# Kernel tuning notes

Hardware: AMD Instinct MI355X
Metric: run time of the kernel (lower is better)

Reference implementation:

```python
import jax, jax.numpy as jnp
import numpy as np

N = 131072          # batch of (action, condition) pairs
ACT_D = 12          # action_dim
COND_D = 256        # condition_dim
K = 256             # num_embeddings (codebook size)
E = 16              # embedding_dim
H1, H2 = 512, 256   # encoder_hidden_dims
COMMIT = 0.25       # commitment_cost
EPS_NORM = 1e-12    # F.normalize eps


def _normalize(x):
    n = jnp.linalg.norm(x, axis=-1, keepdims=True)
    return x / jnp.maximum(n, EPS_NORM)


def setup_inputs() -> dict:
    key = jax.random.key(0)
    ks = jax.random.split(key, 16)
    s = 0.02
    return {
        "actions": jax.random.normal(ks[0], (N, ACT_D), jnp.float32),
        "conditions": jax.random.normal(ks[1], (N, COND_D), jnp.float32),
        # encoder: (COND_D+ACT_D) -> H1 -> H2 -> E  (weights stored [in, out])
        "enc_w1": jax.random.normal(ks[2], (COND_D + ACT_D, H1), jnp.float32) * s,
        "enc_b1": jnp.zeros((H1,), jnp.float32),
        "enc_w2": jax.random.normal(ks[3], (H1, H2), jnp.float32) * s,
        "enc_b2": jnp.zeros((H2,), jnp.float32),
        "enc_w3": jax.random.normal(ks[4], (H2, E), jnp.float32) * s,
        "enc_b3": jnp.zeros((E,), jnp.float32),
        # decoder: (COND_D+E) -> H2 -> H1 -> ACT_D
        "dec_w1": jax.random.normal(ks[5], (COND_D + E, H2), jnp.float32) * s,
        "dec_b1": jnp.zeros((H2,), jnp.float32),
        "dec_w2": jax.random.normal(ks[6], (H2, H1), jnp.float32) * s,
        "dec_b2": jnp.zeros((H1,), jnp.float32),
        "dec_w3": jax.random.normal(ks[7], (H1, ACT_D), jnp.float32) * s,
        "dec_b3": jnp.zeros((ACT_D,), jnp.float32),
        # codebook, init U(-1/K, 1/K) like nn.Embedding in the module
        "embedding": jax.random.uniform(ks[8], (K, E), jnp.float32, -1.0 / K, 1.0 / K),
    }


def reference(actions, conditions, enc_w1, enc_b1, enc_w2, enc_b2, enc_w3, enc_b3,
              dec_w1, dec_b1, dec_w2, dec_b2, dec_w3, dec_b3, embedding):
    sg = jax.lax.stop_gradient
    elu = jax.nn.elu

    # ---- encoder ----
    x = jnp.concatenate([actions, conditions], axis=-1)          # [N, ACT_D+COND_D]
    h = elu(x @ enc_w1 + enc_b1)
    h = elu(h @ enc_w2 + enc_b2)
    z = h @ enc_w3 + enc_b3                                      # [N, E]

    # ---- vector quantizer (distance='cos') ----
    normed_in = sg(_normalize(z))                                # inputs.detach()
    normed_w = _normalize(embedding)
    distances = normed_in @ normed_w.T                           # [N, K] cosine sims

    idx = jnp.argmax(distances, axis=-1)                         # [N]
    quantized = embedding[idx]                                   # one-hot @ codebook == gather

    e_latent_loss = COMMIT * jnp.mean((sg(quantized) - z) ** 2)
    q_latent_loss = jnp.mean((quantized - sg(z)) ** 2)
    quantized_st = z + sg(quantized - z)                         # straight-through

    counts = jnp.zeros((K,), distances.dtype).at[idx].add(1.0)
    avg_probs = counts / N                                       # mean of one-hot encodings
    perplexity = jnp.exp(-jnp.sum(avg_probs * jnp.log(avg_probs + 1e-10)))

    # ---- contrastive loss (training branch, deterministic part) ----
    sortd = jnp.sort(distances, axis=0)                          # ascending per codeword
    n_pos = max(1, N // K)
    dis_pos = jnp.mean(sortd[-n_pos:, :], axis=0, keepdims=True) # [1, K] hardest positives
    dis_neg = sortd[: N // 2, :]                                 # [N//2, K]
    dis = jnp.concatenate([dis_pos, dis_neg], axis=0).T / 0.07   # [K, 1+N//2]
    # cross-entropy with target class 0
    contra_loss = jnp.mean(jax.nn.logsumexp(dis, axis=1) - dis[:, 0])

    # ---- decoder ----
    d = jnp.concatenate([quantized_st, conditions], axis=-1)     # [N, E+COND_D]
    d = elu(d @ dec_w1 + dec_b1)
    d = elu(d @ dec_w2 + dec_b2)
    reconstructed = d @ dec_w3 + dec_b3                          # [N, ACT_D]

    reconstruction_loss = jnp.mean((reconstructed - actions) ** 2)

    return (reconstructed, quantized_st, idx.astype(jnp.int32), q_latent_loss,
            e_latent_loss, contra_loss, perplexity, reconstruction_loss)
```

## Files before the change

kernel.cpp:

```cpp
#include <hip/hip_runtime.h>
#include <hip/hip_bf16.h>
#include <math.h>

#define NROWS 131072
#define ACT_D 12
#define COND_D 256
#define KEMB 256
#define EDIM 16
#define H1D 512
#define H2D 256
#define NB 16384

typedef __attribute__((ext_vector_type(8))) _Float16 half8;
typedef __attribute__((ext_vector_type(4))) float floatx4;
typedef unsigned short ushort_t;

#define LO_SCALE 4096.0f
#define INV_LO_SCALE 2.44140625e-4f


__global__ void init_kernel(int* counts, float* outScal) {
    int t = threadIdx.x;
    counts[t] = 0;
    if (t < 5) outScal[t] = 0.0f;
}

__device__ inline ushort_t f16bits(_Float16 h) { return __builtin_bit_cast(ushort_t, h); }
__device__ inline float f16pair(ushort_t a, ushort_t b) {
    return (float)__builtin_bit_cast(_Float16, a)
         + (float)__builtin_bit_cast(_Float16, b) * INV_LO_SCALE;
}
__device__ inline void splitf(float v, ushort_t& hi, ushort_t& lo) {
    _Float16 h = (_Float16)v;
    _Float16 l = (_Float16)((v - (float)h) * LO_SCALE);
    hi = f16bits(h); lo = f16bits(l);
}

__device__ inline void gload_lds16(const void* g, void* lds) {
    __builtin_amdgcn_global_load_lds((const __attribute__((address_space(1))) void*)g,
                                     (__attribute__((address_space(3))) void*)lds, 16, 0, 0);
}

__global__ __launch_bounds__(256)
void convw_kernel(const float* __restrict__ W, ushort_t* __restrict__ Whi,
                  ushort_t* __restrict__ Wlo, int K, int N, int Kp)
{
    int n = blockIdx.x;
    int k = blockIdx.y * 256 + threadIdx.x;
    if (k >= Kp) return;
    float v = (k < K) ? W[(long)k * N + n] : 0.0f;
    ushort_t h, l; splitf(v, h, l);
    Whi[(long)n * Kp + k] = h;
    Wlo[(long)n * Kp + k] = l;
}

template<int CONCAT>
__global__ __launch_bounds__(256)
void gemm_f16x3_kernel(const void* A0v, const void* A1v,
                       const ushort_t* __restrict__ Bhi, const ushort_t* __restrict__ Blo,
                       const float* __restrict__ bias,
                       ushort_t* __restrict__ Chi, ushort_t* __restrict__ Clo,
                       int Nw, int Kp, int Kvalid)
{
    __shared__ uint lds[8192];
    const int tid = threadIdx.x;
    const int w = tid >> 6, l = tid & 63;
    const int quad = l >> 4, lr = l & 15;
    const long rowBase = (long)blockIdx.x * 128;
    const int colBase = blockIdx.y * 128;
    const int mQ = (w & 1) * 64, nQ = (w >> 1) * 64;

    floatx4 accH[4][4], accX[4][4];
#pragma unroll
    for (int i = 0; i < 4; ++i)
#pragma unroll
        for (int j = 0; j < 4; ++j) { accH[i][j] = (floatx4)(0.0f); accX[i][j] = (floatx4)(0.0f); }

    const int kTiles = Kp / 32;
    for (int t = 0; t < kTiles; ++t) {
        const int k0 = t * 32;
        {
            const ushort_t* src = (w < 2) ? Bhi : Blo;
            uint* dstBase = &lds[(w < 2) ? 4096 : 6144];
            const int j0 = (w & 1) * 4;
#pragma unroll
            for (int j = 0; j < 4; ++j) {
                int jj = j0 + j;
                const ushort_t* g = src + (long)(colBase + jj * 16 + (l >> 2)) * Kp
                                        + k0 + (l & 3) * 8;
                gload_lds16(g, &dstBase[jj * 256]);
            }
        }
        if (CONCAT == 0) {
            const ushort_t* src = (w < 2) ? (const ushort_t*)A0v : (const ushort_t*)A1v;
            uint* dstBase = &lds[(w < 2) ? 0 : 2048];
            const int j0 = (w & 1) * 4;
#pragma unroll
            for (int j = 0; j < 4; ++j) {
                int jj = j0 + j;
                const ushort_t* g = src + (rowBase + jj * 16 + (l >> 2)) * Kp
                                        + k0 + (l & 3) * 8;
                gload_lds16(g, &dstBase[jj * 256]);
            }
        } else {
            const float* A1 = (const float*)A0v;
            const float* A2 = (const float*)A1v;
            const int r = tid >> 1;
            const long grow = rowBase + r;
            const int segBase = (tid & 1) * 2;
#pragma unroll
            for (int s = 0; s < 2; ++s) {
                int seg = segBase + s;
                int kk = k0 + seg * 8;
                float v[8];
                if (kk >= CONCAT && kk + 8 <= Kvalid) {
                    const float* p = A2 + grow * COND_D + (kk - CONCAT);
                    *(float4*)&v[0] = *(const float4*)p;
                    *(float4*)&v[4] = *(const float4*)(p + 4);
                } else if (kk + 8 <= CONCAT) {
                    const float* p = A1 + grow * CONCAT + kk;
                    *(float4*)&v[0] = *(const float4*)p;
                    *(float4*)&v[4] = *(const float4*)(p + 4);
                } else {
#pragma unroll
                    for (int i = 0; i < 8; ++i) {
                        int k = kk + i;
                        v[i] = (k < CONCAT) ? A1[grow * CONCAT + k]
                             : (k < Kvalid) ? A2[grow * COND_D + (k - CONCAT)] : 0.0f;
                    }
                }
                uint hh[4], ll[4];
#pragma unroll
                for (int i = 0; i < 4; ++i) {
                    ushort_t h0, l0, h1, l1;
                    splitf(v[2 * i], h0, l0);
                    splitf(v[2 * i + 1], h1, l1);
                    hh[i] = (uint)h0 | ((uint)h1 << 16);
                    ll[i] = (uint)l0 | ((uint)l1 << 16);
                }
                int dst = r * 16 + seg * 4;
                *(uint4*)&lds[dst]        = *(uint4*)hh;
                *(uint4*)&lds[2048 + dst] = *(uint4*)ll;
            }
        }
        __syncthreads();

#pragma unroll
        for (int jn = 0; jn < 4; ++jn) {
            int boff = (nQ + jn * 16 + lr) * 16 + quad * 4;
            half8 bh = __builtin_bit_cast(half8, *(uint4*)&lds[4096 + boff]);
            half8 bl = __builtin_bit_cast(half8, *(uint4*)&lds[6144 + boff]);
#pragma unroll
            for (int im = 0; im < 4; ++im) {
                int aoff = (mQ + im * 16 + lr) * 16 + quad * 4;
                half8 ah = __builtin_bit_cast(half8, *(uint4*)&lds[aoff]);
                half8 al = __builtin_bit_cast(half8, *(uint4*)&lds[2048 + aoff]);
                accH[im][jn] = __builtin_amdgcn_mfma_f32_16x16x32_f16(ah, bh, accH[im][jn], 0, 0, 0);
                accX[im][jn] = __builtin_amdgcn_mfma_f32_16x16x32_f16(ah, bl, accX[im][jn], 0, 0, 0);
                accX[im][jn] = __builtin_amdgcn_mfma_f32_16x16x32_f16(al, bh, accX[im][jn], 0, 0, 0);
            }
        }
        __syncthreads();
    }

    float bv[4];
#pragma unroll
    for (int jn = 0; jn < 4; ++jn) bv[jn] = bias[colBase + nQ + jn * 16 + lr];
#pragma unroll
    for (int im = 0; im < 4; ++im) {
#pragma unroll
        for (int jn = 0; jn < 4; ++jn) {
            int n = colBase + nQ + jn * 16 + lr;
#pragma unroll
            for (int rr = 0; rr < 4; ++rr) {
                long m = rowBase + mQ + im * 16 + quad * 4 + rr;
                float x = accH[im][jn][rr] + accX[im][jn][rr] * INV_LO_SCALE + bv[jn];
                x = x > 0.0f ? x : (expf(x) - 1.0f);
                ushort_t h, lo; splitf(x, h, lo);
                long idx = m * Nw + n;
                Chi[idx] = h;
                Clo[idx] = lo;
            }
        }
    }
}

__global__ __launch_bounds__(256)
void quantize_kernel(const ushort_t* __restrict__ h2hi, const ushort_t* __restrict__ h2lo,
                     const float* __restrict__ W3,
                     const float* __restrict__ b3, const float* __restrict__ emb,
                     float* __restrict__ distT, float* __restrict__ outQ,
                     float* __restrict__ outIdx, int* __restrict__ counts,
                     float* __restrict__ qsum)
{
    __shared__ float h2t[16 * 260];
    __shared__ float w3t[16 * 260];
    __shared__ float nwt[256 * 20];
    __shared__ float zt[16 * 17];
    __shared__ float dt[16 * 257];
    __shared__ int   lcnt[256];
    __shared__ float swred[4];

    int t = threadIdx.x;
    long rowBase = (long)blockIdx.x * 16;

    for (int it = 0; it < 16; ++it) {
        long idx = (rowBase + it) * 256 + t;
        h2t[it * 260 + t] = f16pair(h2hi[idx], h2lo[idx]);
    }
    for (int it = 0; it < 16; ++it) {
        int flat = it * 256 + t;
        int j = flat >> 4, c = flat & 15;
        w3t[c * 260 + j] = W3[flat];
    }
    {
        float e0[16]; float ss = 0.f;
#pragma unroll
        for (int i = 0; i < 16; ++i) { e0[i] = emb[t * 16 + i]; ss += e0[i] * e0[i]; }
        float inv = 1.0f / fmaxf(sqrtf(ss), 1e-12f);
#pragma unroll
        for (int i = 0; i < 16; ++i) nwt[t * 20 + i] = e0[i] * inv;
    }
    lcnt[t] = 0;
    __syncthreads();

    int r = t >> 4, c = t & 15;
    float zacc = b3[c];
    for (int j4 = 0; j4 < 64; ++j4) {
        float4 h = *(const float4*)&h2t[r * 260 + j4 * 4];
        float4 w = *(const float4*)&w3t[c * 260 + j4 * 4];
        zacc += h.x * w.x + h.y * w.y + h.z * w.z + h.w * w.w;
    }
    float ss = zacc * zacc;
#pragma unroll
    for (int m = 1; m < 16; m <<= 1) ss += __shfl_xor(ss, m, 64);
    zt[r * 17 + c] = zacc / fmaxf(sqrtf(ss), 1e-12f);
    __syncthreads();

    float zr[16];
#pragma unroll
    for (int e = 0; e < 16; ++e) zr[e] = zt[r * 17 + e];
    float best = -1e30f; int bidx = 0;
    for (int cc = 0; cc < 16; ++cc) {
        int col = cc * 16 + c;
        float d = 0.f;
#pragma unroll
        for (int e4 = 0; e4 < 4; ++e4) {
            float4 wv = *(const float4*)&nwt[col * 20 + e4 * 4];
            d += zr[e4 * 4 + 0] * wv.x + zr[e4 * 4 + 1] * wv.y
               + zr[e4 * 4 + 2] * wv.z + zr[e4 * 4 + 3] * wv.w;
        }
        dt[r * 257 + col] = d;
        if (d > best || (d == best && col < bidx)) { best = d; bidx = col; }
    }
#pragma unroll
    for (int m = 1; m < 16; m <<= 1) {
        float ov = __shfl_xor(best, m, 64);
        int   oi = __shfl_xor(bidx, m, 64);
        if (ov > best || (ov == best && oi < bidx)) { best = ov; bidx = oi; }
    }

    float q = emb[bidx * 16 + c];
    outQ[(rowBase + r) * 16 + c] = q;
    float df = q - zacc;
    float part = df * df;
#pragma unroll
    for (int m = 1; m < 64; m <<= 1) part += __shfl_xor(part, m, 64);
    if ((t & 63) == 0) swred[t >> 6] = part;
    if (c == 0) {
        outIdx[rowBase + r] = (float)bidx;
        atomicAdd(&lcnt[bidx], 1);
    }
    __syncthreads();
    if (t == 0) atomicAdd(qsum, swred[0] + swred[1] + swred[2] + swred[3]);
    if (lcnt[t] > 0) atomicAdd(&counts[t], lcnt[t]);

    int rr = t & 15, cg = t >> 4;
    for (int i = 0; i < 16; ++i) {
        int col = i * 16 + cg;
        distT[(long)col * NROWS + rowBase + rr] = dt[rr * 257 + col];
    }
}

__global__ __launch_bounds__(1024)
void selA_kernel(const float* __restrict__ distT, int* __restrict__ stats)
{
    __shared__ int hist[NB];
    __shared__ int part[1024];
    int t = threadIdx.x, c = blockIdx.x;
    for (int i = t; i < NB; i += 1024) hist[i] = 0;
    __syncthreads();
    const float* col = distT + (long)c * NROWS;
    for (int i = t; i < NROWS; i += 1024) {
        float v = col[i];
        int b = (int)((v + 1.0f) * (NB * 0.5f));
        b = min(max(b, 0), NB - 1);
        atomicAdd(&hist[b], 1);
    }
    __syncthreads();
    const int CH = NB / 1024;
    int s = 0;
    for (int i = 0; i < CH; ++i) s += hist[t * CH + i];
    part[t] = s;
    __syncthreads();
    if (t == 0) {
        int target = NROWS / 2;
        int cum = 0; int chunk = 0;
        while (cum + part[chunk] < target) { cum += part[chunk]; ++chunk; }
        int b = chunk * CH;
        while (cum + hist[b] < target) { cum += hist[b]; ++b; }
        int medBin = b, needLow = target - cum, cntMed = hist[b];
        int cumA = 0; chunk = 1023;
        while (cumA + part[chunk] < 512) { cumA += part[chunk]; --chunk; }
        b = chunk * CH + CH - 1;
        while (cumA + hist[b] < 512) { cumA += hist[b]; --b; }
        int topBin = b, needTop = 512 - cumA, cntTop = hist[b];
        int* st = stats + c * 6;
        st[0] = medBin; st[1] = needLow; st[2] = cntMed;
        st[3] = topBin; st[4] = needTop; st[5] = cntTop;
    }
}

__global__ __launch_bounds__(1024)
void selB_kernel(const float* __restrict__ distT, const int* __restrict__ stats,
                 float* __restrict__ contra_sum)
{
    __shared__ float red[64];
    int t = threadIdx.x, c = blockIdx.x;
    const int* st = stats + c * 6;
    int medBin = st[0], needLow = st[1], cntMed = st[2];
    int topBin = st[3], needTop = st[4], cntTop = st[5];
    const float binw = 2.0f / NB;
    float mUp = -1.0f + (medBin + 1) * binw;
    const float INVT = 1.0f / 0.07f;
    const float* col = distT + (long)c * NROWS;
    float topS = 0.f, tbS = 0.f, lowS = 0.f, mbS = 0.f;
    for (int i = t; i < NROWS; i += 1024) {
        float v = col[i];
        int b = (int)((v + 1.0f) * (NB * 0.5f));
        b = min(max(b, 0), NB - 1);
        if (b > topBin)       topS += v;
        else if (b == topBin) tbS += v;
        if (b < medBin)       lowS += expf((v - mUp) * INVT);
        else if (b == medBin) mbS  += expf((v - mUp) * INVT);
    }
#pragma unroll
    for (int m = 1; m < 64; m <<= 1) {
        topS += __shfl_xor(topS, m, 64);
        tbS  += __shfl_xor(tbS, m, 64);
        lowS += __shfl_xor(lowS, m, 64);
        mbS  += __shfl_xor(mbS, m, 64);
    }
    if ((t & 63) == 0) {
        int wv = t >> 6;
        red[wv * 4 + 0] = topS; red[wv * 4 + 1] = tbS;
        red[wv * 4 + 2] = lowS; red[wv * 4 + 3] = mbS;
    }
    __syncthreads();
    if (t == 0) {
        float T0 = 0, T1 = 0, T2 = 0, T3 = 0;
        for (int wv = 0; wv < 16; ++wv) {
            T0 += red[wv * 4 + 0]; T1 += red[wv * 4 + 1];
            T2 += red[wv * 4 + 2]; T3 += red[wv * 4 + 3];
        }
        float dis_pos = (T0 + needTop * (T1 / cntTop)) * (1.0f / 512.0f);
        float S = T2 + needLow * (T3 / cntMed);
        float colContra = log1pf(S * expf((mUp - dis_pos) * INVT));
        atomicAdd(contra_sum, colContra);
    }
}

__global__ __launch_bounds__(256)
void dec3_kernel(const ushort_t* __restrict__ d2hi, const ushort_t* __restrict__ d2lo,
                 const float* __restrict__ W,
                 const float* __restrict__ bias, const float* __restrict__ actions,
                 float* __restrict__ rec, float* __restrict__ recon_sum)
{
    __shared__ float dtile[16 * 516];
    __shared__ float wt[512 * 12];
    __shared__ float red2[4];
    int t = threadIdx.x;
    long rowBase = (long)blockIdx.x * 16;
    for (int it = 0; it < 24; ++it) wt[it * 256 + t] = W[it * 256 + t];
    for (int it = 0; it < 32; ++it) {
        int flat = it * 256 + t;
        int r = flat >> 9, k = flat & 511;
        long idx = (rowBase + r) * 512 + k;
        dtile[r * 516 + k] = f16pair(d2hi[idx], d2lo[idx]);
    }
    __syncthreads();
    float part = 0.f;
    if (t < 192) {
        int r = t / 12, cc = t % 12;
        float acc = bias[cc];
        for (int k4 = 0; k4 < 128; ++k4) {
            float4 h = *(const float4*)&dtile[r * 516 + k4 * 4];
            acc += h.x * wt[(k4 * 4 + 0) * 12 + cc] + h.y * wt[(k4 * 4 + 1) * 12 + cc]
                 + h.z * wt[(k4 * 4 + 2) * 12 + cc] + h.w * wt[(k4 * 4 + 3) * 12 + cc];
        }
        rec[(rowBase + r) * 12 + cc] = acc;
        float df = acc - actions[(rowBase + r) * 12 + cc];
        part = df * df;
    }
#pragma unroll
    for (int m = 1; m < 64; m <<= 1) part += __shfl_xor(part, m, 64);
    if ((t & 63) == 0) red2[t >> 6] = part;
    __syncthreads();
    if (t == 0) atomicAdd(recon_sum, red2[0] + red2[1] + red2[2] + red2[3]);
}

__global__ void finalize_kernel(const int* __restrict__ counts, float* __restrict__ outScal)
{
    __shared__ float red[4];
    int t = threadIdx.x;
    float p = counts[t] * (1.0f / NROWS);
    float term = p * logf(p + 1e-10f);
#pragma unroll
    for (int m = 1; m < 64; m <<= 1) term += __shfl_xor(term, m, 64);
    if ((t & 63) == 0) red[t >> 6] = term;
    __syncthreads();
    if (t == 0) {
        float hsum = red[0] + red[1] + red[2] + red[3];
        float qsum = outScal[0], contra = outScal[2], recon = outScal[4];
        float ql = qsum * (1.0f / (NROWS * 16.0f));
        outScal[0] = ql;
        outScal[1] = 0.25f * ql;
        outScal[2] = contra * (1.0f / 256.0f);
        outScal[3] = expf(-hsum);
        outScal[4] = recon * (1.0f / (NROWS * 12.0f));
    }
}

extern "C" void kernel_launch(void* const* d_in, const int* in_sizes, int n_in,
                              void* d_out, int out_size, void* d_ws, size_t ws_size,
                              hipStream_t stream)
{
    const float* actions    = (const float*)d_in[0];
    const float* conditions = (const float*)d_in[1];
    const float* enc_w1 = (const float*)d_in[2];
    const float* enc_b1 = (const float*)d_in[3];
    const float* enc_w2 = (const float*)d_in[4];
    const float* enc_b2 = (const float*)d_in[5];
    const float* enc_w3 = (const float*)d_in[6];
    const float* enc_b3 = (const float*)d_in[7];
    const float* dec_w1 = (const float*)d_in[8];
    const float* dec_b1 = (const float*)d_in[9];
    const float* dec_w2 = (const float*)d_in[10];
    const float* dec_b2 = (const float*)d_in[11];
    const float* dec_w3 = (const float*)d_in[12];
    const float* dec_b3 = (const float*)d_in[13];
    const float* emb    = (const float*)d_in[14];

    float* out     = (float*)d_out;
    float* outRec  = out;
    float* outQ    = out + (long)NROWS * 12;
    float* outIdx  = out + (long)NROWS * 28;
    float* outScal = out + (long)NROWS * 29;

    ushort_t* wb    = (ushort_t*)d_out;
    ushort_t* w1hi  = wb;            ushort_t* w1lo  = wb + 147456;
    ushort_t* w2hi  = wb + 294912;   ushort_t* w2lo  = wb + 425984;
    ushort_t* wd1hi = wb + 557056;   ushort_t* wd1lo = wb + 630784;
    ushort_t* wd2hi = wb + 704512;   ushort_t* wd2lo = wb + 835584;

    float* ws = (float*)d_ws;
    int* counts = (int*)ws;
    int* stats  = (int*)(ws + 256);
    ushort_t* h2hi = (ushort_t*)(ws + 1792);
    ushort_t* h2lo = (ushort_t*)(ws + 16779008);
    ushort_t* d1hi = h2hi;
    ushort_t* d1lo = h2lo;
    float*    P1   = ws + 33556224;
    ushort_t* h1hi = (ushort_t*)P1;
    ushort_t* h1lo = (ushort_t*)(ws + 67110656);
    float*    distT = P1;
    ushort_t* d2hi = h1hi;
    ushort_t* d2lo = h1lo;

    hipLaunchKernelGGL(init_kernel, dim3(1), dim3(256), 0, stream, counts, outScal);
    hipLaunchKernelGGL(convw_kernel, dim3(512, 2), dim3(256), 0, stream, enc_w1, w1hi, w1lo, 268, 512, 288);
    hipLaunchKernelGGL(convw_kernel, dim3(256, 2), dim3(256), 0, stream, enc_w2, w2hi, w2lo, 512, 256, 512);
    hipLaunchKernelGGL(convw_kernel, dim3(256, 2), dim3(256), 0, stream, dec_w1, wd1hi, wd1lo, 272, 256, 288);
    hipLaunchKernelGGL(convw_kernel, dim3(512, 1), dim3(256), 0, stream, dec_w2, wd2hi, wd2lo, 256, 512, 256);
    hipLaunchKernelGGL((gemm_f16x3_kernel<ACT_D>), dim3(1024, 4), dim3(256), 0, stream,
                       (const void*)actions, (const void*)conditions, w1hi, w1lo, enc_b1,
                       h1hi, h1lo, H1D, 288, 268);
    hipLaunchKernelGGL((gemm_f16x3_kernel<0>), dim3(1024, 2), dim3(256), 0, stream,
                       (const void*)h1hi, (const void*)h1lo, w2hi, w2lo, enc_b2,
                       h2hi, h2lo, H2D, 512, 512);
    hipLaunchKernelGGL(quantize_kernel, dim3(8192), dim3(256), 0, stream,
                       h2hi, h2lo, enc_w3, enc_b3, emb, distT, outQ, outIdx, counts, &outScal[0]);
    hipLaunchKernelGGL(selA_kernel, dim3(256), dim3(1024), 0, stream, distT, stats);
    hipLaunchKernelGGL(selB_kernel, dim3(256), dim3(1024), 0, stream, distT, stats, &outScal[2]);
    hipLaunchKernelGGL((gemm_f16x3_kernel<EDIM>), dim3(1024, 2), dim3(256), 0, stream,
                       (const void*)outQ, (const void*)conditions, wd1hi, wd1lo, dec_b1,
                       d1hi, d1lo, H2D, 288, 272);
    hipLaunchKernelGGL((gemm_f16x3_kernel<0>), dim3(1024, 4), dim3(256), 0, stream,
                       (const void*)d1hi, (const void*)d1lo, wd2hi, wd2lo, dec_b2,
                       d2hi, d2lo, H1D, 256, 256);
    hipLaunchKernelGGL(dec3_kernel, dim3(8192), dim3(256), 0, stream,
                       d2hi, d2lo, dec_w3, dec_b3, actions, outRec, &outScal[4]);
    hipLaunchKernelGGL(finalize_kernel, dim3(1), dim3(256), 0, stream, counts, outScal);
}
```

Measured before the change: 1.714 ms.

## Double-buffer GEMM LDS tiles and shrink row tile to 64 for occupancy

Restructures the split-f16 GEMM to use a 64x128 block tile with each wave owning 32 columns, double-buffered LDS staging so the next k-tile loads while MFMAs run on the current one, and launch bounds requesting 3 blocks per CU. The grid doubles in row blocks to cover the same rows. This aims to hide global load latency and the per-tile sync stall and to raise occupancy. The cost is more B-tile reloads per output row and more LDS per block.

Result: faster. 1.566 ms (-8.6%).

```diff
diff --git a/kernel.cpp b/kernel.cpp
--- a/kernel.cpp
+++ b/kernel.cpp
@@ -55,125 +55,126 @@
 }
 
 template<int CONCAT>
-__global__ __launch_bounds__(256)
+__global__ __launch_bounds__(256, 3)
 void gemm_f16x3_kernel(const void* A0v, const void* A1v,
                        const ushort_t* __restrict__ Bhi, const ushort_t* __restrict__ Blo,
                        const float* __restrict__ bias,
                        ushort_t* __restrict__ Chi, ushort_t* __restrict__ Clo,
                        int Nw, int Kp, int Kvalid)
 {
-    __shared__ uint lds[8192];
+    __shared__ uint lds[12288];
     const int tid = threadIdx.x;
     const int w = tid >> 6, l = tid & 63;
     const int quad = l >> 4, lr = l & 15;
-    const long rowBase = (long)blockIdx.x * 128;
+    const long rowBase = (long)blockIdx.x * 64;
     const int colBase = blockIdx.y * 128;
-    const int mQ = (w & 1) * 64, nQ = (w >> 1) * 64;
-
-    floatx4 accH[4][4], accX[4][4];
+    const int nQ = w * 32;
+
+    floatx4 accH[4][2], accX[4][2];
 #pragma unroll
     for (int i = 0; i < 4; ++i)
 #pragma unroll
-        for (int j = 0; j < 4; ++j) { accH[i][j] = (floatx4)(0.0f); accX[i][j] = (floatx4)(0.0f); }
-
-    const int kTiles = Kp / 32;
-    for (int t = 0; t < kTiles; ++t) {
-        const int k0 = t * 32;
-        {
-            const ushort_t* src = (w < 2) ? Bhi : Blo;
-            uint* dstBase = &lds[(w < 2) ? 4096 : 6144];
-            const int j0 = (w & 1) * 4;
-#pragma unroll
-            for (int j = 0; j < 4; ++j) {
-                int jj = j0 + j;
-                const ushort_t* g = src + (long)(colBase + jj * 16 + (l >> 2)) * Kp
-                                        + k0 + (l & 3) * 8;
-                gload_lds16(g, &dstBase[jj * 256]);
-            }
+        for (int j = 0; j < 2; ++j) { accH[i][j] = (floatx4)(0.0f); accX[i][j] = (floatx4)(0.0f); }
+
+    auto stage = [&](int buf, int k0) {
+        const int base = buf * 6144;
+#pragma unroll
+        for (int h = 0; h < 2; ++h) {
+            const ushort_t* g = Bhi + (long)(colBase + h * 64 + l) * Kp + k0 + w * 8;
+            gload_lds16(g, &lds[base + 2048 + w * 512 + h * 256]);
+        }
+#pragma unroll
+        for (int h = 0; h < 2; ++h) {
+            const ushort_t* g = Blo + (long)(colBase + h * 64 + l) * Kp + k0 + w * 8;
+            gload_lds16(g, &lds[base + 4096 + w * 512 + h * 256]);
         }
         if (CONCAT == 0) {
-            const ushort_t* src = (w < 2) ? (const ushort_t*)A0v : (const ushort_t*)A1v;
-            uint* dstBase = &lds[(w < 2) ? 0 : 2048];
-            const int j0 = (w & 1) * 4;
-#pragma unroll
-            for (int j = 0; j < 4; ++j) {
-                int jj = j0 + j;
-                const ushort_t* g = src + (rowBase + jj * 16 + (l >> 2)) * Kp
-                                        + k0 + (l & 3) * 8;
-                gload_lds16(g, &dstBase[jj * 256]);
-            }
+            const ushort_t* gh = (const ushort_t*)A0v + (rowBase + l) * Kp + k0 + w * 8;
+            gload_lds16(gh, &lds[base + w * 256]);
+            const ushort_t* gl = (const ushort_t*)A1v + (rowBase + l) * Kp + k0 + w * 8;
+            gload_lds16(gl, &lds[base + 1024 + w * 256]);
         } else {
             const float* A1 = (const float*)A0v;
             const float* A2 = (const float*)A1v;
-            const int r = tid >> 1;
-            const long grow = rowBase + r;
-            const int segBase = (tid & 1) * 2;
-#pragma unroll
-            for (int s = 0; s < 2; ++s) {
-                int seg = segBase + s;
-                int kk = k0 + seg * 8;
-                float v[8];
-                if (kk >= CONCAT && kk + 8 <= Kvalid) {
-                    const float* p = A2 + grow * COND_D + (kk - CONCAT);
-                    *(float4*)&v[0] = *(const float4*)p;
-                    *(float4*)&v[4] = *(const float4*)(p + 4);
-                } else if (kk + 8 <= CONCAT) {
-                    const float* p = A1 + grow * CONCAT + kk;
-                    *(float4*)&v[0] = *(const float4*)p;
-                    *(float4*)&v[4] = *(const float4*)(p + 4);
-                } else {
-#pragma unroll
-                    for (int i = 0; i < 8; ++i) {
-                        int k = kk + i;
-                        v[i] = (k < CONCAT) ? A1[grow * CONCAT + k]
-                             : (k < Kvalid) ? A2[grow * COND_D + (k - CONCAT)] : 0.0f;
-                    }
+            const long grow = rowBase + l;
+            const int kk = k0 + w * 8;
+            float v[8];
+            if (kk >= CONCAT && kk + 8 <= Kvalid) {
+                const float* p = A2 + grow * COND_D + (kk - CONCAT);
+                *(float4*)&v[0] = *(const float4*)p;
+                *(float4*)&v[4] = *(const float4*)(p + 4);
+            } else if (kk + 8 <= CONCAT) {
+                const float* p = A1 + grow * CONCAT + kk;
+                *(float4*)&v[0] = *(const float4*)p;
+                *(float4*)&v[4] = *(const float4*)(p + 4);
+            } else {
+#pragma unroll
+                for (int i = 0; i < 8; ++i) {
+                    int k = kk + i;
+                    v[i] = (k < CONCAT) ? A1[grow * CONCAT + k]
+                         : (k < Kvalid) ? A2[grow * COND_D + (k - CONCAT)] : 0.0f;
                 }
-                uint hh[4], ll[4];
-#pragma unroll
-                for (int i = 0; i < 4; ++i) {
-                    ushort_t h0, l0, h1, l1;
-                    splitf(v[2 * i], h0, l0);
-                    splitf(v[2 * i + 1], h1, l1);
-                    hh[i] = (uint)h0 | ((uint)h1 << 16);
-                    ll[i] = (uint)l0 | ((uint)l1 << 16);
-                }
-                int dst = r * 16 + seg * 4;
-                *(uint4*)&lds[dst]        = *(uint4*)hh;
-                *(uint4*)&lds[2048 + dst] = *(uint4*)ll;
             }
-        }
+            uint hh[4], ll[4];
+#pragma unroll
+            for (int i = 0; i < 4; ++i) {
+                ushort_t h0, l0, h1, l1;
+                splitf(v[2 * i], h0, l0);
+                splitf(v[2 * i + 1], h1, l1);
+                hh[i] = (uint)h0 | ((uint)h1 << 16);
+                ll[i] = (uint)l0 | ((uint)l1 << 16);
+            }
+            *(uint4*)&lds[base + w * 256 + l * 4]        = *(uint4*)hh;
+            *(uint4*)&lds[base + 1024 + w * 256 + l * 4] = *(uint4*)ll;
+        }
+    };
+
+    auto compute = [&](int buf) {
+        const int base = buf * 6144;
+        half8 bh[2], bl[2];
+#pragma unroll
+        for (int jn = 0; jn < 2; ++jn) {
+            int boff = base + 2048 + quad * 512 + (nQ + jn * 16 + lr) * 4;
+            bh[jn] = __builtin_bit_cast(half8, *(uint4*)&lds[boff]);
+            bl[jn] = __builtin_bit_cast(half8, *(uint4*)&lds[boff + 2048]);
+        }
+#pragma unroll
+        for (int im = 0; im < 4; ++im) {
+            int aoff = base + quad * 256 + (im * 16 + lr) * 4;
+            half8 ah = __builtin_bit_cast(half8, *(uint4*)&lds[aoff]);
+            half8 al = __builtin_bit_cast(half8, *(uint4*)&lds[aoff + 1024]);
+#pragma unroll
+            for (int jn = 0; jn < 2; ++jn) {
+                accH[im][jn] = __builtin_amdgcn_mfma_f32_16x16x32_f16(ah, bh[jn], accH[im][jn], 0, 0, 0);
+                accX[im][jn] = __builtin_amdgcn_mfma_f32_16x16x32_f16(ah, bl[jn], accX[im][jn], 0, 0, 0);
+                accX[im][jn] = __builtin_amdgcn_mfma_f32_16x16x32_f16(al, bh[jn], accX[im][jn], 0, 0, 0);
+            }
+        }
+    };
+
+    const int kTiles = Kp / 32;
+    stage(0, 0);
+    __syncthreads();
+    int cur = 0;
+    for (int t = 0; t < kTiles - 1; ++t) {
+        stage(cur ^ 1, (t + 1) * 32);
+        compute(cur);
         __syncthreads();
-
-#pragma unroll
-        for (int jn = 0; jn < 4; ++jn) {
-            int boff = (nQ + jn * 16 + lr) * 16 + quad * 4;
-            half8 bh = __builtin_bit_cast(half8, *(uint4*)&lds[4096 + boff]);
-            half8 bl = __builtin_bit_cast(half8, *(uint4*)&lds[6144 + boff]);
-#pragma unroll
-            for (int im = 0; im < 4; ++im) {
-                int aoff = (mQ + im * 16 + lr) * 16 + quad * 4;
-                half8 ah = __builtin_bit_cast(half8, *(uint4*)&lds[aoff]);
-                half8 al = __builtin_bit_cast(half8, *(uint4*)&lds[2048 + aoff]);
-                accH[im][jn] = __builtin_amdgcn_mfma_f32_16x16x32_f16(ah, bh, accH[im][jn], 0, 0, 0);
-                accX[im][jn] = __builtin_amdgcn_mfma_f32_16x16x32_f16(ah, bl, accX[im][jn], 0, 0, 0);
-                accX[im][jn] = __builtin_amdgcn_mfma_f32_16x16x32_f16(al, bh, accX[im][jn], 0, 0, 0);
-            }
-        }
-        __syncthreads();
-    }
-
-    float bv[4];
-#pragma unroll
-    for (int jn = 0; jn < 4; ++jn) bv[jn] = bias[colBase + nQ + jn * 16 + lr];
+        cur ^= 1;
+    }
+    compute(cur);
+
+    float bv[2];
+#pragma unroll
+    for (int jn = 0; jn < 2; ++jn) bv[jn] = bias[colBase + nQ + jn * 16 + lr];
 #pragma unroll
     for (int im = 0; im < 4; ++im) {
 #pragma unroll
-        for (int jn = 0; jn < 4; ++jn) {
+        for (int jn = 0; jn < 2; ++jn) {
             int n = colBase + nQ + jn * 16 + lr;
 #pragma unroll
             for (int rr = 0; rr < 4; ++rr) {
-                long m = rowBase + mQ + im * 16 + quad * 4 + rr;
+                long m = rowBase + im * 16 + quad * 4 + rr;
                 float x = accH[im][jn][rr] + accX[im][jn][rr] * INV_LO_SCALE + bv[jn];
                 x = x > 0.0f ? x : (expf(x) - 1.0f);
                 ushort_t h, lo; splitf(x, h, lo);
@@ -482,20 +483,20 @@
     hipLaunchKernelGGL(convw_kernel, dim3(256, 2), dim3(256), 0, stream, enc_w2, w2hi, w2lo, 512, 256, 512);
     hipLaunchKernelGGL(convw_kernel, dim3(256, 2), dim3(256), 0, stream, dec_w1, wd1hi, wd1lo, 272, 256, 288);
     hipLaunchKernelGGL(convw_kernel, dim3(512, 1), dim3(256), 0, stream, dec_w2, wd2hi, wd2lo, 256, 512, 256);
-    hipLaunchKernelGGL((gemm_f16x3_kernel<ACT_D>), dim3(1024, 4), dim3(256), 0, stream,
+    hipLaunchKernelGGL((gemm_f16x3_kernel<ACT_D>), dim3(2048, 4), dim3(256), 0, stream,
                        (const void*)actions, (const void*)conditions, w1hi, w1lo, enc_b1,
                        h1hi, h1lo, H1D, 288, 268);
-    hipLaunchKernelGGL((gemm_f16x3_kernel<0>), dim3(1024, 2), dim3(256), 0, stream,
+    hipLaunchKernelGGL((gemm_f16x3_kernel<0>), dim3(2048, 2), dim3(256), 0, stream,
                        (const void*)h1hi, (const void*)h1lo, w2hi, w2lo, enc_b2,
                        h2hi, h2lo, H2D, 512, 512);
     hipLaunchKernelGGL(quantize_kernel, dim3(8192), dim3(256), 0, stream,
                        h2hi, h2lo, enc_w3, enc_b3, emb, distT, outQ, outIdx, counts, &outScal[0]);
     hipLaunchKernelGGL(selA_kernel, dim3(256), dim3(1024), 0, stream, distT, stats);
     hipLaunchKernelGGL(selB_kernel, dim3(256), dim3(1024), 0, stream, distT, stats, &outScal[2]);
-    hipLaunchKernelGGL((gemm_f16x3_kernel<EDIM>), dim3(1024, 2), dim3(256), 0, stream,
+    hipLaunchKernelGGL((gemm_f16x3_kernel<EDIM>), dim3(2048, 2), dim3(256), 0, stream,
                        (const void*)outQ, (const void*)conditions, wd1hi, wd1lo, dec_b1,
                        d1hi, d1lo, H2D, 288, 272);
-    hipLaunchKernelGGL((gemm_f16x3_kernel<0>), dim3(1024, 4), dim3(256), 0, stream,
+    hipLaunchKernelGGL((gemm_f16x3_kernel<0>), dim3(2048, 4), dim3(256), 0, stream,
                        (const void*)d1hi, (const void*)d1lo, wd2hi, wd2lo, dec_b2,
                        d2hi, d2lo, H1D, 256, 256);
     hipLaunchKernelGGL(dec3_kernel, dim3(8192), dim3(256), 0, stream,
```
